# Performance work log

Measured on AMD Instinct MI355X. Metric: run time of the kernel, lower is better.

The kernel has to match this reference:

```python
import jax, jax.numpy as jnp
import numpy as np

BETA = 0.25
SCALE_NUM = 4  # len(latents_scale)


def setup_inputs() -> dict:
    key = jax.random.key(0)
    kz, ke = jax.random.split(key)
    z = jax.random.normal(kz, (8, 256, 32, 32), dtype=jnp.float32)
    emb_weight = jax.random.normal(ke, (16384, 256), dtype=jnp.float32) * 0.02
    return {"z": z, "emb_weight": emb_weight}


def reference(z, emb_weight):
    # z: [B, C, H, W] with C == vq_embed_dim and H == W (source reshapes with W twice)
    B, C, H, W = z.shape
    z_det = jax.lax.stop_gradient(z)

    # NOTE: in the source, `residual` is flattened ONCE before the scale loop and
    # never updated inside it, so every scale picks the same indices. We compute
    # the nearest-codebook assignment once (identical math, argmin of cdist is
    # invariant under sqrt, so squared distances suffice).
    residual = jnp.transpose(z_det, (0, 2, 3, 1)).reshape(-1, C)  # [N, D], N=B*H*W
    d2 = (jnp.sum(residual * residual, axis=1, keepdims=True)
          - 2.0 * residual @ emb_weight.T
          + jnp.sum(emb_weight * emb_weight, axis=1))  # [N, n_e]
    idx = jnp.argmin(d2, axis=1).reshape(B, W, W)  # [B, W, W]

    quantized = jnp.transpose(emb_weight[idx], (0, 3, 1, 2))  # [B, C, H, W]

    z_hat = jnp.zeros_like(z_det)
    loss = jnp.float32(0.0)
    for _ in range(SCALE_NUM):
        z_hat = z_hat + quantized
        loss = loss + BETA * jnp.mean((jax.lax.stop_gradient(z_hat) - z) ** 2) \
                    + jnp.mean((z_hat - z_det) ** 2)
    loss = loss / SCALE_NUM

    total_idx = jnp.concatenate([idx] * SCALE_NUM, axis=1)  # [B, SCALE_NUM*W, W]
    z_hat_out = z + jax.lax.stop_gradient(z_hat - z)  # straight-through
    return z_hat_out, loss, total_idx
```

## Files before the change

### kernel.cpp

```cpp
#include <hip/hip_runtime.h>

#define D      256
#define N_E    16384
#define NPTS   8192
#define ZOUT   2097152
#define MARGIN 2.0e-2f
#define STRIPS 4
#define ECH    17

typedef short bf16x8 __attribute__((ext_vector_type(8)));
typedef unsigned short us8 __attribute__((ext_vector_type(8)));
typedef float f32x16 __attribute__((ext_vector_type(16)));
typedef unsigned long long u64;

__device__ __forceinline__ unsigned short f2bf(float x) {
    unsigned int u = __float_as_uint(x);
    return (unsigned short)((u + 0x7FFFu + ((u >> 16) & 1u)) >> 16);
}
__device__ __forceinline__ float bf2f(unsigned short h) {
    return __uint_as_float((unsigned int)h << 16);
}
__device__ __forceinline__ void gl_lds16(const void* g, void* l) {
    __builtin_amdgcn_global_load_lds(
        (const __attribute__((address_space(1))) unsigned int*)g,
        (__attribute__((address_space(3))) unsigned int*)l, 16, 0, 0);
}

__global__ __launch_bounds__(256) void prep(
    const float* __restrict__ z, const float* __restrict__ emb,
    unsigned short* __restrict__ Zpk, unsigned short* __restrict__ Epk,
    float* __restrict__ e2, float* __restrict__ loss) {
    __shared__ float sh[32];
    const int t = threadIdx.x;
    if (blockIdx.x == 0 && t == 0) loss[0] = 0.f;
    if (blockIdx.x < 256) {
        const int n0 = blockIdx.x * 32;
        const int p = t & 31, ks8 = t >> 5;
        const int n = n0 + p;
        const int b = n >> 10, hw = n & 1023;
        const float* zb = z + (size_t)b * 262144 + hw;
        const int k0 = ks8 * 32;
        float v[32];
        #pragma unroll
        for (int kk = 0; kk < 32; ++kk)
            v[kk] = zb[(size_t)(k0 + kk) * 1024];
        const int g = n >> 5;
        #pragma unroll
        for (int i = 0; i < 4; ++i) {
            us8 hv;
            #pragma unroll
            for (int c = 0; c < 8; ++c) hv[c] = f2bf(-2.0f * v[i * 8 + c]);
            const int kabs = k0 + i * 8;
            const int ks = kabs >> 4;
            const int l = (n & 31) + ((kabs >> 3) & 1) * 32;
            *(us8*)(Zpk + ((size_t)(g * 16 + ks) * 64 + l) * 8) = hv;
        }
    } else {
        const int bi = blockIdx.x - 256;
        const int j0 = bi * 32;
        const int jj = j0 + (t >> 3), q = t & 7;
        const float* row = emb + (size_t)jj * D + q * 32;
        float v[32];
        float s = 0.f;
        #pragma unroll
        for (int i = 0; i < 8; ++i) {
            const float4 x = *(const float4*)(row + i * 4);
            v[i * 4] = x.x; v[i * 4 + 1] = x.y; v[i * 4 + 2] = x.z; v[i * 4 + 3] = x.w;
            s += x.x * x.x + x.y * x.y + x.z * x.z + x.w * x.w;
        }
        #pragma unroll
        for (int i = 0; i < 4; ++i) {
            us8 hv;
            #pragma unroll
            for (int c = 0; c < 8; ++c) hv[c] = f2bf(v[i * 8 + c]);
            const int kabs = q * 32 + i * 8;
            const int ks = kabs >> 4;
            const int l = (jj & 31) + ((kabs >> 3) & 1) * 32;
            *(us8*)(Epk + ((size_t)(bi * ECH + ks) * 64 + l) * 8) = hv;
        }
        s += __shfl_xor(s, 1);
        s += __shfl_xor(s, 2);
        s += __shfl_xor(s, 4);
        if (q == 0) { e2[jj] = s; sh[t >> 3] = s; }
        __syncthreads();
        if (t < 64) {
            us8 hv;
            #pragma unroll
            for (int c = 0; c < 8; ++c) hv[c] = 0;
            if (t < 32) {
                const float vv = sh[t];
                const unsigned short hi = f2bf(vv);
                hv[0] = hi;
                hv[1] = f2bf(vv - bf2f(hi));
            }
            *(us8*)(Epk + ((size_t)bi * ECH + 16) * 512 + t * 8) = hv;
        }
    }
}

__global__ __launch_bounds__(256, 2) void mfma_gemm(
    const unsigned short* __restrict__ Epk, const unsigned short* __restrict__ Zpk,
    float* __restrict__ tminv, u64* __restrict__ tmask) {
    __shared__ unsigned short Zbuf[64 * 512];

    const int tid = threadIdx.x, lane = tid & 63, wid = tid >> 6;
    const int c32 = lane & 31, l5 = lane >> 5;
    const int n0 = (int)blockIdx.y * 128;
    const int cs0 = (int)blockIdx.x * (STRIPS * 256);

    us8 puu;
    #pragma unroll
    for (int c = 0; c < 8; ++c) puu[c] = 0;
    if (l5 == 0) { puu[0] = 0x3F80; puu[1] = 0x3F80; }
    const bf16x8 pu = (bf16x8)puu;

    #pragma unroll
    for (int ks = 0; ks < 16; ++ks)
        gl_lds16(Zpk + ((size_t)((n0 >> 5) + wid) * 16 + ks) * 512 + lane * 8,
                 Zbuf + (wid * 16 + ks) * 512);
    __syncthreads();

    for (int s = 0; s < STRIPS; ++s) {
        const int cb = cs0 + s * 256 + wid * 64;
        const unsigned short* eb =
            Epk + ((size_t)(cb >> 5) * ECH) * 512 + lane * 8;
        const unsigned short* zb = Zbuf + lane * 8;

        f32x16 acc[2][4];
        const f32x16 z16 = {0.f};
        #pragma unroll
        for (int i = 0; i < 2; ++i)
            #pragma unroll
            for (int j = 0; j < 4; ++j) acc[i][j] = z16;

        bf16x8 eq0a = *(const bf16x8*)(eb);
        bf16x8 eq0b = *(const bf16x8*)(eb + ECH * 512);
        bf16x8 eq1a = *(const bf16x8*)(eb + 512);
        bf16x8 eq1b = *(const bf16x8*)(eb + ECH * 512 + 512);
        bf16x8 pc[4], pn[4];
        #pragma unroll
        for (int j = 0; j < 4; ++j) pc[j] = *(const bf16x8*)(zb + (j * 16) * 512);

        #pragma unroll 4
        for (int ks = 0; ks < 16; ++ks) {
            bf16x8 ef0, ef1;
            if ((ks & 1) == 0) { ef0 = eq0a; ef1 = eq0b; }
            else               { ef0 = eq1a; ef1 = eq1b; }
            if (ks < 15) {
                const unsigned short* ep = eb + (ks + 2) * 512;
                if ((ks & 1) == 0) {
                    eq0a = *(const bf16x8*)ep;
                    eq0b = *(const bf16x8*)(ep + ECH * 512);
                } else {
                    eq1a = *(const bf16x8*)ep;
                    eq1b = *(const bf16x8*)(ep + ECH * 512);
                }
                #pragma unroll
                for (int j = 0; j < 4; ++j)
                    pn[j] = *(const bf16x8*)(zb + (j * 16 + ks + 1) * 512);
            }
            acc[0][0] = __builtin_amdgcn_mfma_f32_32x32x16_bf16(ef0, pc[0], acc[0][0], 0, 0, 0);
            acc[0][1] = __builtin_amdgcn_mfma_f32_32x32x16_bf16(ef0, pc[1], acc[0][1], 0, 0, 0);
            acc[0][2] = __builtin_amdgcn_mfma_f32_32x32x16_bf16(ef0, pc[2], acc[0][2], 0, 0, 0);
            acc[0][3] = __builtin_amdgcn_mfma_f32_32x32x16_bf16(ef0, pc[3], acc[0][3], 0, 0, 0);
            acc[1][0] = __builtin_amdgcn_mfma_f32_32x32x16_bf16(ef1, pc[0], acc[1][0], 0, 0, 0);
            acc[1][1] = __builtin_amdgcn_mfma_f32_32x32x16_bf16(ef1, pc[1], acc[1][1], 0, 0, 0);
            acc[1][2] = __builtin_amdgcn_mfma_f32_32x32x16_bf16(ef1, pc[2], acc[1][2], 0, 0, 0);
            acc[1][3] = __builtin_amdgcn_mfma_f32_32x32x16_bf16(ef1, pc[3], acc[1][3], 0, 0, 0);
            if (ks < 15) {
                #pragma unroll
                for (int j = 0; j < 4; ++j) pc[j] = pn[j];
            }
        }
        #pragma unroll
        for (int j = 0; j < 4; ++j) {
            acc[0][j] = __builtin_amdgcn_mfma_f32_32x32x16_bf16(eq0a, pu, acc[0][j], 0, 0, 0);
            acc[1][j] = __builtin_amdgcn_mfma_f32_32x32x16_bf16(eq0b, pu, acc[1][j], 0, 0, 0);
        }

        #pragma unroll
        for (int j = 0; j < 4; ++j) {
            float m = acc[0][j][0];
            #pragma unroll
            for (int r = 1; r < 16; ++r) m = fminf(m, acc[0][j][r]);
            #pragma unroll
            for (int r = 0; r < 16; ++r) m = fminf(m, acc[1][j][r]);
            m = fminf(m, __shfl_xor(m, 32));
            const float th = m + MARGIN;
            unsigned mk[2];
            #pragma unroll
            for (int i = 0; i < 2; ++i) {
                unsigned mm = 0;
                #pragma unroll
                for (int r = 0; r < 16; ++r) {
                    const int row = (r & 3) + 8 * (r >> 2) + 4 * l5;
                    mm |= (acc[i][j][r] <= th) ? (1u << row) : 0u;
                }
                mk[i] = mm | (unsigned)__shfl_xor((int)mm, 32);
            }
            if (l5 == 0) {
                const size_t pt = (size_t)(n0 + j * 32 + c32);
                tminv[pt * 256 + (cb >> 6)] = m;
                tmask[pt * 256 + (cb >> 6)] = ((u64)mk[1] << 32) | (u64)mk[0];
            }
        }
    }
}

__global__ __launch_bounds__(1024) void rescore_quant(
    const float* __restrict__ tminv, const u64* __restrict__ tmask,
    const float* __restrict__ emb, const float* __restrict__ e2,
    const float* __restrict__ z, float* __restrict__ out,
    float* __restrict__ out_idx, float* __restrict__ loss) {
    __shared__ float smz[32][257];
    __shared__ int idx_s[32];
    __shared__ float wsum[16];
    const int tid = threadIdx.x, lane = tid & 63, wd = tid >> 6;
    const int n0 = blockIdx.x * 32;
    const int b = n0 >> 10, hw0 = n0 & 1023;

    #pragma unroll
    for (int pass = 0; pass < 8; ++pass) {
        const int c = pass * 32 + (tid >> 5);
        const int hw = tid & 31;
        smz[hw][c] = z[(size_t)b * 262144 + (size_t)c * 1024 + hw0 + hw];
    }
    __syncthreads();

    #pragma unroll 1
    for (int p = 0; p < 2; ++p) {
        const int lp = wd * 2 + p;
        const int n = n0 + lp;
        const float* zrow = smz[lp];
        const float4 zr = {zrow[lane * 4], zrow[lane * 4 + 1],
                           zrow[lane * 4 + 2], zrow[lane * 4 + 3]};
        const float4 tv = *(const float4*)(tminv + (size_t)n * 256 + lane * 4);

        float m1 = fminf(fminf(tv.x, tv.y), fminf(tv.z, tv.w));
        #pragma unroll
        for (int st = 1; st < 64; st <<= 1) m1 = fminf(m1, __shfl_xor(m1, st));
        const float thresh = m1 + MARGIN;

        u64 best = ~0ull;
        const float tva[4] = {tv.x, tv.y, tv.z, tv.w};
        #pragma unroll
        for (int k = 0; k < 4; ++k) {
            u64 gm = __ballot(tva[k] <= thresh);
            while (gm) {
                const int bit = (int)__builtin_ctzll(gm);
                gm &= gm - 1;
                const int g = bit * 4 + k;
                u64 cm = tmask[(size_t)n * 256 + g];
                while (cm) {
                    const int r = (int)__builtin_ctzll(cm);
                    cm &= cm - 1;
                    const int c = g * 64 + r;
                    const float4 ev = *(const float4*)(emb + (size_t)c * D + lane * 4);
                    float s = zr.x * ev.x + zr.y * ev.y + zr.z * ev.z + zr.w * ev.w;
                    #pragma unroll
                    for (int st = 1; st < 64; st <<= 1) s += __shfl_xor(s, st);
                    const float d = e2[c] - 2.0f * s;
                    unsigned int u = __float_as_uint(d);
                    u = (u & 0x80000000u) ? ~u : (u | 0x80000000u);
                    const u64 key = ((u64)u << 32) | (unsigned int)c;
                    if (key < best) best = key;
                }
            }
        }
        if (lane == 0)
            idx_s[lp] = (int)(unsigned int)(best & 0xFFFFFFFFull);
    }
    __syncthreads();

    if (tid < 32) {
        const float fv = (float)idx_s[tid];
        #pragma unroll
        for (int sc = 0; sc < 4; ++sc)
            out_idx[b * 4096 + sc * 1024 + hw0 + tid] = fv;
    }
    const int hw_l = tid & 31, cg = tid >> 5;
    const int j = idx_s[hw_l];
    const float* er = emb + (size_t)j * D + cg * 8;
    const float4 q0 = *(const float4*)er;
    const float4 q1 = *(const float4*)(er + 4);
    const float qv[8] = {q0.x, q0.y, q0.z, q0.w, q1.x, q1.y, q1.z, q1.w};
    float e = 0.f;
    #pragma unroll
    for (int cc = 0; cc < 8; ++cc) {
        const int c = cg * 8 + cc;
        const size_t zi = (size_t)b * 262144 + (size_t)c * 1024 + hw0 + hw_l;
        const float zv = smz[hw_l][c];
        const float q = qv[cc];
        const float zh = ((q + q) + q) + q;
        out[zi] = zv + (zh - zv);
        e += 30.0f * q * q - 20.0f * q * zv + 4.0f * zv * zv;
    }
    #pragma unroll
    for (int off = 32; off > 0; off >>= 1) e += __shfl_down(e, off);
    if (lane == 0) wsum[wd] = e;
    __syncthreads();
    if (tid == 0) {
        float s = 0.f;
        #pragma unroll
        for (int i = 0; i < 16; ++i) s += wsum[i];
        atomicAdd(loss, s * (0.3125f / 2097152.0f));
    }
}

extern "C" void kernel_launch(void* const* d_in, const int* in_sizes, int n_in,
                              void* d_out, int out_size, void* d_ws, size_t ws_size,
                              hipStream_t stream) {
    const float* z = (const float*)d_in[0];
    const float* emb = (const float*)d_in[1];
    float* out = (float*)d_out;

    unsigned short* Zpk = (unsigned short*)d_ws;
    unsigned short* Epk = Zpk + (size_t)NPTS * D;
    float* e2 = (float*)(Epk + (size_t)(N_E / 32) * ECH * 512);
    float* tminv = e2 + N_E;
    u64* tmask = (u64*)(tminv + (size_t)NPTS * 256);

    float* loss = out + ZOUT;
    float* out_idx = out + ZOUT + 1;

    prep<<<768, 256, 0, stream>>>(z, emb, Zpk, Epk, e2, loss);
    mfma_gemm<<<dim3(N_E / (256 * STRIPS), NPTS / 128), 256, 0, stream>>>(
        Epk, Zpk, tminv, tmask);
    rescore_quant<<<256, 1024, 0, stream>>>(tminv, tmask, emb, e2, z,
                                            out, out_idx, loss);
}
```

Baseline: 159.8 us.

## Restructure MFMA GEMM into 1024-thread blocks with per-wave point-group split

The distance GEMM block grows from 4 to 16 waves. Each wave now owns one 32-point group and 128 codewords per strip, instead of all 128 points and 64 codewords. The block covers 4096 codewords across 8 strips, so the grid shrinks to 4x64 blocks and the Z tile in LDS is shared by more waves. The point is to cut per-wave register pressure and increase codebook reuse per block, at the cost of loading more E fragments per MFMA and possibly leaving fewer blocks to fill the CUs.

```diff
diff --git a/kernel.cpp b/kernel.cpp
--- a/kernel.cpp
+++ b/kernel.cpp
@@ -5,7 +5,7 @@
 #define NPTS   8192
 #define ZOUT   2097152
 #define MARGIN 2.0e-2f
-#define STRIPS 4
+#define STRIPS 8
 #define ECH    17
 
 typedef short bf16x8 __attribute__((ext_vector_type(8)));
@@ -98,15 +98,16 @@
     }
 }
 
-__global__ __launch_bounds__(256, 2) void mfma_gemm(
+__global__ __launch_bounds__(1024) void mfma_gemm(
     const unsigned short* __restrict__ Epk, const unsigned short* __restrict__ Zpk,
     float* __restrict__ tminv, u64* __restrict__ tmask) {
     __shared__ unsigned short Zbuf[64 * 512];
 
     const int tid = threadIdx.x, lane = tid & 63, wid = tid >> 6;
     const int c32 = lane & 31, l5 = lane >> 5;
+    const int cc = wid & 3, pg = wid >> 2;
     const int n0 = (int)blockIdx.y * 128;
-    const int cs0 = (int)blockIdx.x * (STRIPS * 256);
+    const int cs0 = (int)blockIdx.x * (STRIPS * 512);
 
     us8 puu;
     #pragma unroll
@@ -115,76 +116,58 @@
     const bf16x8 pu = (bf16x8)puu;
 
     #pragma unroll
-    for (int ks = 0; ks < 16; ++ks)
-        gl_lds16(Zpk + ((size_t)((n0 >> 5) + wid) * 16 + ks) * 512 + lane * 8,
-                 Zbuf + (wid * 16 + ks) * 512);
+    for (int i = 0; i < 4; ++i) {
+        const int ch = wid * 4 + i;
+        gl_lds16(Zpk + ((size_t)((n0 >> 5) + (ch >> 4)) * 16 + (ch & 15)) * 512
+                     + lane * 8,
+                 Zbuf + ch * 512);
+    }
     __syncthreads();
 
+    const unsigned short* zb = Zbuf + (pg * 16) * 512 + lane * 8;
+
     for (int s = 0; s < STRIPS; ++s) {
-        const int cb = cs0 + s * 256 + wid * 64;
+        const int cb = cs0 + s * 512 + cc * 128;
         const unsigned short* eb =
             Epk + ((size_t)(cb >> 5) * ECH) * 512 + lane * 8;
-        const unsigned short* zb = Zbuf + lane * 8;
-
-        f32x16 acc[2][4];
+
+        f32x16 acc[4];
         const f32x16 z16 = {0.f};
         #pragma unroll
-        for (int i = 0; i < 2; ++i)
-            #pragma unroll
-            for (int j = 0; j < 4; ++j) acc[i][j] = z16;
-
-        bf16x8 eq0a = *(const bf16x8*)(eb);
-        bf16x8 eq0b = *(const bf16x8*)(eb + ECH * 512);
-        bf16x8 eq1a = *(const bf16x8*)(eb + 512);
-        bf16x8 eq1b = *(const bf16x8*)(eb + ECH * 512 + 512);
-        bf16x8 pc[4], pn[4];
-        #pragma unroll
-        for (int j = 0; j < 4; ++j) pc[j] = *(const bf16x8*)(zb + (j * 16) * 512);
+        for (int f = 0; f < 4; ++f) acc[f] = z16;
+
+        bf16x8 ec[4], en[4];
+        #pragma unroll
+        for (int f = 0; f < 4; ++f)
+            ec[f] = *(const bf16x8*)(eb + (f * ECH + 0) * 512);
+        bf16x8 pc = *(const bf16x8*)(zb);
+        bf16x8 pn;
 
         #pragma unroll 4
         for (int ks = 0; ks < 16; ++ks) {
-            bf16x8 ef0, ef1;
-            if ((ks & 1) == 0) { ef0 = eq0a; ef1 = eq0b; }
-            else               { ef0 = eq1a; ef1 = eq1b; }
-            if (ks < 15) {
-                const unsigned short* ep = eb + (ks + 2) * 512;
-                if ((ks & 1) == 0) {
-                    eq0a = *(const bf16x8*)ep;
-                    eq0b = *(const bf16x8*)(ep + ECH * 512);
-                } else {
-                    eq1a = *(const bf16x8*)ep;
-                    eq1b = *(const bf16x8*)(ep + ECH * 512);
-                }
-                #pragma unroll
-                for (int j = 0; j < 4; ++j)
-                    pn[j] = *(const bf16x8*)(zb + (j * 16 + ks + 1) * 512);
-            }
-            acc[0][0] = __builtin_amdgcn_mfma_f32_32x32x16_bf16(ef0, pc[0], acc[0][0], 0, 0, 0);
-            acc[0][1] = __builtin_amdgcn_mfma_f32_32x32x16_bf16(ef0, pc[1], acc[0][1], 0, 0, 0);
-            acc[0][2] = __builtin_amdgcn_mfma_f32_32x32x16_bf16(ef0, pc[2], acc[0][2], 0, 0, 0);
-            acc[0][3] = __builtin_amdgcn_mfma_f32_32x32x16_bf16(ef0, pc[3], acc[0][3], 0, 0, 0);
-            acc[1][0] = __builtin_amdgcn_mfma_f32_32x32x16_bf16(ef1, pc[0], acc[1][0], 0, 0, 0);
-            acc[1][1] = __builtin_amdgcn_mfma_f32_32x32x16_bf16(ef1, pc[1], acc[1][1], 0, 0, 0);
-            acc[1][2] = __builtin_amdgcn_mfma_f32_32x32x16_bf16(ef1, pc[2], acc[1][2], 0, 0, 0);
-            acc[1][3] = __builtin_amdgcn_mfma_f32_32x32x16_bf16(ef1, pc[3], acc[1][3], 0, 0, 0);
-            if (ks < 15) {
-                #pragma unroll
-                for (int j = 0; j < 4; ++j) pc[j] = pn[j];
-            }
-        }
-        #pragma unroll
-        for (int j = 0; j < 4; ++j) {
-            acc[0][j] = __builtin_amdgcn_mfma_f32_32x32x16_bf16(eq0a, pu, acc[0][j], 0, 0, 0);
-            acc[1][j] = __builtin_amdgcn_mfma_f32_32x32x16_bf16(eq0b, pu, acc[1][j], 0, 0, 0);
-        }
-
-        #pragma unroll
-        for (int j = 0; j < 4; ++j) {
-            float m = acc[0][j][0];
-            #pragma unroll
-            for (int r = 1; r < 16; ++r) m = fminf(m, acc[0][j][r]);
-            #pragma unroll
-            for (int r = 0; r < 16; ++r) m = fminf(m, acc[1][j][r]);
+            #pragma unroll
+            for (int f = 0; f < 4; ++f)
+                en[f] = *(const bf16x8*)(eb + (f * ECH + ks + 1) * 512);
+            if (ks < 15) pn = *(const bf16x8*)(zb + (ks + 1) * 512);
+            acc[0] = __builtin_amdgcn_mfma_f32_32x32x16_bf16(ec[0], pc, acc[0], 0, 0, 0);
+            acc[1] = __builtin_amdgcn_mfma_f32_32x32x16_bf16(ec[1], pc, acc[1], 0, 0, 0);
+            acc[2] = __builtin_amdgcn_mfma_f32_32x32x16_bf16(ec[2], pc, acc[2], 0, 0, 0);
+            acc[3] = __builtin_amdgcn_mfma_f32_32x32x16_bf16(ec[3], pc, acc[3], 0, 0, 0);
+            #pragma unroll
+            for (int f = 0; f < 4; ++f) ec[f] = en[f];
+            if (ks < 15) pc = pn;
+        }
+        #pragma unroll
+        for (int f = 0; f < 4; ++f)
+            acc[f] = __builtin_amdgcn_mfma_f32_32x32x16_bf16(ec[f], pu, acc[f], 0, 0, 0);
+
+        #pragma unroll
+        for (int gi = 0; gi < 2; ++gi) {
+            float m = acc[2 * gi][0];
+            #pragma unroll
+            for (int r = 1; r < 16; ++r) m = fminf(m, acc[2 * gi][r]);
+            #pragma unroll
+            for (int r = 0; r < 16; ++r) m = fminf(m, acc[2 * gi + 1][r]);
             m = fminf(m, __shfl_xor(m, 32));
             const float th = m + MARGIN;
             unsigned mk[2];
@@ -194,14 +177,15 @@
                 #pragma unroll
                 for (int r = 0; r < 16; ++r) {
                     const int row = (r & 3) + 8 * (r >> 2) + 4 * l5;
-                    mm |= (acc[i][j][r] <= th) ? (1u << row) : 0u;
+                    mm |= (acc[2 * gi + i][r] <= th) ? (1u << row) : 0u;
                 }
                 mk[i] = mm | (unsigned)__shfl_xor((int)mm, 32);
             }
             if (l5 == 0) {
-                const size_t pt = (size_t)(n0 + j * 32 + c32);
-                tminv[pt * 256 + (cb >> 6)] = m;
-                tmask[pt * 256 + (cb >> 6)] = ((u64)mk[1] << 32) | (u64)mk[0];
+                const size_t pt = (size_t)(n0 + pg * 32 + c32);
+                const int g = (cb >> 6) + gi;
+                tminv[pt * 256 + g] = m;
+                tmask[pt * 256 + g] = ((u64)mk[1] << 32) | (u64)mk[0];
             }
         }
     }
@@ -324,7 +308,7 @@
     float* out_idx = out + ZOUT + 1;
 
     prep<<<768, 256, 0, stream>>>(z, emb, Zpk, Epk, e2, loss);
-    mfma_gemm<<<dim3(N_E / (256 * STRIPS), NPTS / 128), 256, 0, stream>>>(
+    mfma_gemm<<<dim3(N_E / (STRIPS * 512), NPTS / 128), 1024, 0, stream>>>(
         Epk, Zpk, tminv, tmask);
     rescore_quant<<<256, 1024, 0, stream>>>(tminv, tmask, emb, e2, z,
                                             out, out_idx, loss);
```

Measured after the change: 204.5 us. 1.28x slower.
